# Optimization experiments

Measured on AMD Instinct MI355X. Metric: run time of the kernel, lower is better.

## Reference

```python
import jax, jax.numpy as jnp
import numpy as np

N_NODES = 100000
N_EDGES = 1600000
DIM = 3
HID = 128
BN_EPS = 1e-5


def _bn(x, g, b):
    # BatchNorm1d, training-mode batch statistics (biased variance, like torch)
    m = jnp.mean(x, axis=0)
    v = jnp.var(x, axis=0)
    return (x - m) * jax.lax.rsqrt(v + BN_EPS) * g + b


def _gin_mlp(h, w1, b1, g1, be1, w2, b2, g2, be2, w3, b3):
    # Linear -> BN -> ReLU -> (Dropout: identity in eval) -> Linear -> BN -> ReLU -> Linear
    h = jax.nn.relu(_bn(h @ w1 + b1, g1, be1))
    h = jax.nn.relu(_bn(h @ w2 + b2, g2, be2))
    return h @ w3 + b3


def _gin_conv(x, src, dst, eps, mlp_params):
    # GINConv: mlp((1+eps)*x_i + sum_{j->i} x_j); scatter-add over edge targets
    agg = jax.ops.segment_sum(x[src], dst, num_segments=N_NODES)
    return _gin_mlp((1.0 + eps) * x + agg, *mlp_params)


def setup_inputs() -> dict:
    key = jax.random.key(0)
    ks = jax.random.split(key, 32)

    def w(k, shape, scale=0.05):
        return jax.random.normal(k, shape, dtype=jnp.float32) * scale

    inp = {}
    inp["coords"] = jax.random.normal(ks[0], (N_NODES, DIM), dtype=jnp.float32)
    inp["edge_index"] = jax.random.randint(ks[1], (2, N_EDGES), 0, N_NODES, dtype=jnp.int32)

    # GIN layer 0 MLP (dim -> hid -> hid -> hid)
    inp["g0_w1"] = w(ks[2], (DIM, HID)); inp["g0_b1"] = jnp.zeros((HID,), jnp.float32)
    inp["g0_g1"] = jnp.ones((HID,), jnp.float32); inp["g0_be1"] = jnp.zeros((HID,), jnp.float32)
    inp["g0_w2"] = w(ks[3], (HID, HID)); inp["g0_b2"] = jnp.zeros((HID,), jnp.float32)
    inp["g0_g2"] = jnp.ones((HID,), jnp.float32); inp["g0_be2"] = jnp.zeros((HID,), jnp.float32)
    inp["g0_w3"] = w(ks[4], (HID, HID)); inp["g0_b3"] = jnp.zeros((HID,), jnp.float32)
    inp["eps0"] = jnp.zeros((), jnp.float32)
    inp["bn0_g"] = jnp.ones((HID,), jnp.float32); inp["bn0_b"] = jnp.zeros((HID,), jnp.float32)

    # GIN layer 1 MLP (hid -> hid -> hid -> hid)
    inp["g1_w1"] = w(ks[5], (HID, HID)); inp["g1_b1"] = jnp.zeros((HID,), jnp.float32)
    inp["g1_g1"] = jnp.ones((HID,), jnp.float32); inp["g1_be1"] = jnp.zeros((HID,), jnp.float32)
    inp["g1_w2"] = w(ks[6], (HID, HID)); inp["g1_b2"] = jnp.zeros((HID,), jnp.float32)
    inp["g1_g2"] = jnp.ones((HID,), jnp.float32); inp["g1_be2"] = jnp.zeros((HID,), jnp.float32)
    inp["g1_w3"] = w(ks[7], (HID, HID)); inp["g1_b3"] = jnp.zeros((HID,), jnp.float32)
    inp["eps1"] = jnp.zeros((), jnp.float32)
    inp["bn1_g"] = jnp.ones((HID,), jnp.float32); inp["bn1_b"] = jnp.zeros((HID,), jnp.float32)

    # decoder MLP: (2*hid+1) -> hid -> hid//2 -> 1, sigmoid
    inp["d_w1"] = w(ks[8], (2 * HID + 1, HID)); inp["d_b1"] = jnp.zeros((HID,), jnp.float32)
    inp["d_g"] = jnp.ones((HID,), jnp.float32); inp["d_be"] = jnp.zeros((HID,), jnp.float32)
    inp["d_w2"] = w(ks[9], (HID, HID // 2)); inp["d_b2"] = jnp.zeros((HID // 2,), jnp.float32)
    inp["d_w3"] = w(ks[10], (HID // 2, 1)); inp["d_b3"] = jnp.zeros((1,), jnp.float32)
    return inp


def reference(coords, edge_index,
              g0_w1, g0_b1, g0_g1, g0_be1, g0_w2, g0_b2, g0_g2, g0_be2, g0_w3, g0_b3, eps0, bn0_g, bn0_b,
              g1_w1, g1_b1, g1_g1, g1_be1, g1_w2, g1_b2, g1_g2, g1_be2, g1_w3, g1_b3, eps1, bn1_g, bn1_b,
              d_w1, d_b1, d_g, d_be, d_w2, d_b2, d_w3, d_b3):
    node_0 = edge_index[0]
    node_1 = edge_index[1]

    mlp0 = (g0_w1, g0_b1, g0_g1, g0_be1, g0_w2, g0_b2, g0_g2, g0_be2, g0_w3, g0_b3)
    mlp1 = (g1_w1, g1_b1, g1_g1, g1_be1, g1_w2, g1_b2, g1_g2, g1_be2, g1_w3, g1_b3)

    x = _gin_conv(coords, node_0, node_1, eps0, mlp0)
    x = jax.nn.relu(_bn(x, bn0_g, bn0_b))
    x = _gin_conv(x, node_0, node_1, eps1, mlp1)
    x = jax.nn.relu(_bn(x, bn1_g, bn1_b))

    # edge_l_cntr branch: per-edge contour-length feature + endpoint concat
    l = jnp.linalg.norm(coords[node_1] - coords[node_0], axis=1, keepdims=True)  # [E,1]
    h = jnp.concatenate([x[node_0], x[node_1], l], axis=-1)  # [E, 2*hid+1]

    h = jax.nn.relu(_bn(h @ d_w1 + d_b1, d_g, d_be))
    h = jax.nn.relu(h @ d_w2 + d_b2)
    out = jax.nn.sigmoid((h @ d_w3 + d_b3).squeeze(-1))  # [E]
    return out
```

## Files before the change

kernel.cpp:

```cpp
#include <hip/hip_runtime.h>
#include <hip/hip_bf16.h>
#include <math.h>


typedef __attribute__((ext_vector_type(8))) __bf16 bf16x8;
typedef __attribute__((ext_vector_type(4))) float f32x4;

__device__ __forceinline__ unsigned int pack_bf16(float a, float b) {
    unsigned short ua = __builtin_bit_cast(unsigned short, __float2bfloat16(a));
    unsigned short ub = __builtin_bit_cast(unsigned short, __float2bfloat16(b));
    return (unsigned int)ua | ((unsigned int)ub << 16);
}


__global__ void hist_dst(const int* __restrict__ edst, int* __restrict__ cursor, int E) {
    int e = blockIdx.x * 256 + threadIdx.x;
    if (e < E) atomicAdd(&cursor[edst[e]], 1);
}

__global__ __launch_bounds__(1024) void scan_deg(const int* deg, int* rowoff, int* cursor, int N) {
    __shared__ int sums[1024];
    const int t = threadIdx.x;
    const int chunk = (N + 1023) >> 10;
    int lo = t * chunk, hi = lo + chunk;
    if (lo > N) lo = N;
    if (hi > N) hi = N;
    int s = 0;
    for (int i = lo; i < hi; ++i) s += deg[i];
    sums[t] = s;
    __syncthreads();
    for (int off = 1; off < 1024; off <<= 1) {
        int add = (t >= off) ? sums[t - off] : 0;
        __syncthreads();
        sums[t] += add;
        __syncthreads();
    }
    int run = sums[t] - s;
    for (int i = lo; i < hi; ++i) {
        int d = deg[i];
        rowoff[i] = run;
        cursor[i] = run;
        run += d;
    }
    if (t == 1023) rowoff[N] = sums[1023];
}

__global__ void fill_csr(const int* __restrict__ esrc, const int* __restrict__ edst,
                         const float* __restrict__ coords,
                         int* cursor, int* __restrict__ perm, int* __restrict__ dperm,
                         int* __restrict__ eperm, float* __restrict__ lperm, int E) {
    int e = blockIdx.x * 256 + threadIdx.x;
    if (e >= E) return;
    int s0 = esrc[e], d0 = edst[e];
    int pos = atomicAdd(&cursor[d0], 1);
    perm[pos] = s0;
    dperm[pos] = d0;
    eperm[pos] = e;
    float dx = coords[d0*3+0] - coords[s0*3+0];
    float dy = coords[d0*3+1] - coords[s0*3+1];
    float dz = coords[d0*3+2] - coords[s0*3+2];
    lperm[pos] = sqrtf(dx*dx + dy*dy + dz*dz);
}


__global__ void gather_coords(const float* __restrict__ coords,
                              const int* __restrict__ rowoff, const int* __restrict__ perm,
                              float* __restrict__ agg0, int N) {
    int i = blockIdx.x * 256 + threadIdx.x;
    if (i >= N) return;
    float ax = 0.f, ay = 0.f, az = 0.f;
    int b = rowoff[i], t = rowoff[i+1];
    for (int j = b; j < t; ++j) {
        int p = perm[j];
        ax += coords[p*3+0];
        ay += coords[p*3+1];
        az += coords[p*3+2];
    }
    agg0[i*3+0] = ax; agg0[i*3+1] = ay; agg0[i*3+2] = az;
}

__global__ __launch_bounds__(256) void gather_combine_bn(const float* __restrict__ x,
                                                         const int* __restrict__ rowoff,
                                                         const int* __restrict__ perm,
                                                         const float* __restrict__ sc,
                                                         const float* __restrict__ sh,
                                                         const float* __restrict__ eps,
                                                         float* __restrict__ y, int N) {
    int node = blockIdx.x * 4 + (threadIdx.x >> 6);
    int lane = threadIdx.x & 63;
    if (node >= N) return;
    float ep = 1.f + *eps;
    const float2* x2 = (const float2*)x;
    float2 scv = ((const float2*)sc)[lane];
    float2 shv = ((const float2*)sh)[lane];
    int b = rowoff[node], t = rowoff[node+1];
    float2 acc = make_float2(0.f, 0.f);
    int j = b;
    for (; j + 2 <= t; j += 2) {
        int p0 = perm[j], p1 = perm[j+1];
        float2 v0 = x2[(size_t)p0*64 + lane];
        float2 v1 = x2[(size_t)p1*64 + lane];
        acc.x += fmaxf(fmaf(v0.x, scv.x, shv.x), 0.f) + fmaxf(fmaf(v1.x, scv.x, shv.x), 0.f);
        acc.y += fmaxf(fmaf(v0.y, scv.y, shv.y), 0.f) + fmaxf(fmaf(v1.y, scv.y, shv.y), 0.f);
    }
    if (j < t) {
        int p = perm[j];
        float2 v = x2[(size_t)p*64 + lane];
        acc.x += fmaxf(fmaf(v.x, scv.x, shv.x), 0.f);
        acc.y += fmaxf(fmaf(v.y, scv.y, shv.y), 0.f);
    }
    float2 own = x2[(size_t)node*64 + lane];
    acc.x = fmaf(ep, fmaxf(fmaf(own.x, scv.x, shv.x), 0.f), acc.x);
    acc.y = fmaf(ep, fmaxf(fmaf(own.y, scv.y, shv.y), 0.f), acc.y);
    ((float2*)y)[(size_t)node*64 + lane] = acc;
}


__global__ __launch_bounds__(256) void lin0(const float* __restrict__ coords,
                                            const float* __restrict__ agg0,
                                            const float* __restrict__ W1,
                                            const float* __restrict__ b1,
                                            const float* __restrict__ eps0,
                                            float* __restrict__ t1,
                                            float* __restrict__ stats, int nrows) {
    int col = threadIdx.x & 127, half = threadIdx.x >> 7;
    float w0 = W1[col], w1 = W1[128+col], w2 = W1[256+col], bb = b1[col];
    float ep = 1.f + *eps0;
    float s = 0.f, q = 0.f;
    int r0 = blockIdx.x * 64;
    for (int i = 0; i < 32; ++i) {
        int row = r0 + half + 2*i;
        if (row < nrows) {
            float h0 = fmaf(ep, coords[row*3+0], agg0[row*3+0]);
            float h1 = fmaf(ep, coords[row*3+1], agg0[row*3+1]);
            float h2 = fmaf(ep, coords[row*3+2], agg0[row*3+2]);
            float v = fmaf(h0, w0, fmaf(h1, w1, fmaf(h2, w2, bb)));
            t1[row*128+col] = v;
            s += v; q += v*v;
        }
    }
    __shared__ float red[512];
    red[half*128+col] = s;
    red[256 + half*128+col] = q;
    __syncthreads();
    if (threadIdx.x < 128) {
        atomicAdd(&stats[col],       red[col] + red[128+col]);
        atomicAdd(&stats[128+col],   red[256+col] + red[384+col]);
    }
}

__global__ void bn_fin(const float* __restrict__ stats, const float* __restrict__ g,
                       const float* __restrict__ be, float* __restrict__ sc,
                       float* __restrict__ sh, float inv_count) {
    int c = threadIdx.x;
    float m = stats[c] * inv_count;
    float v = stats[128+c] * inv_count - m*m;
    float a = g[c] * rsqrtf(fmaxf(v, 0.f) + 1e-5f);
    sc[c] = a;
    sh[c] = be[c] - m*a;
}

__global__ void prep_w2(const float* __restrict__ W2, unsigned short* __restrict__ w2t) {
    int i = blockIdx.x * 256 + threadIdx.x;
    if (i >= 128*64) return;
    int k = i >> 6, c = i & 63;
    w2t[c*128 + k] = __builtin_bit_cast(unsigned short, __float2bfloat16(W2[i]));
}

__global__ void prep_wT(const float* __restrict__ w0, const float* __restrict__ w1,
                        const float* __restrict__ w2, const float* __restrict__ w3,
                        const float* __restrict__ w4, const float* __restrict__ w5,
                        const float* __restrict__ w6, unsigned short* __restrict__ dst) {
    int m = blockIdx.y;
    const float* src = (m==0)?w0:(m==1)?w1:(m==2)?w2:(m==3)?w3:(m==4)?w4:(m==5)?w5:w6;
    int i = blockIdx.x * 256 + threadIdx.x;
    int k = i >> 7, c = i & 127;
    dst[m*16384 + c*128 + k] =
        __builtin_bit_cast(unsigned short, __float2bfloat16(src[i]));
}

template<bool IN_BN, bool STATS>
__global__ __launch_bounds__(256) void gemm_mfma(const float* __restrict__ A,
                                                 const unsigned short* __restrict__ wT,
                                                 const float* __restrict__ bias,
                                                 const float* __restrict__ sc,
                                                 const float* __restrict__ sh,
                                                 float* __restrict__ C,
                                                 float* __restrict__ stats, int nrows) {
    __shared__ int4 sAi[1024];
    __shared__ int4 sBi[2048];
    __shared__ float sred[2][4][128];
    char* sA = (char*)sAi;
    char* sB = (char*)sBi;
    const int tid = threadIdx.x;
    const int tile0 = blockIdx.x * 64;

    {
        const int4* src = (const int4*)wT;
        #pragma unroll
        for (int ii = 0; ii < 8; ++ii) {
            int s = tid + 256*ii;
            int col = s >> 4, k16 = s & 15;
            int byte = ((col << 8) + (k16 << 4)) ^ ((col & 7) << 4);
            *(int4*)(sB + byte) = src[s];
        }
    }
    {
        const int c4 = tid & 31;
        const int rb = tid >> 5;
        float4 s4, t4;
        if (IN_BN) {
            s4 = ((const float4*)sc)[c4];
            t4 = ((const float4*)sh)[c4];
        }
        const float4* A4 = (const float4*)A;
        #pragma unroll
        for (int i = 0; i < 8; ++i) {
            int r = rb + 8*i;
            int row = tile0 + r;
            float4 v = make_float4(0.f, 0.f, 0.f, 0.f);
            if (row < nrows) {
                v = A4[(size_t)row*32 + c4];
                if (IN_BN) {
                    v.x = fmaxf(fmaf(v.x, s4.x, t4.x), 0.f);
                    v.y = fmaxf(fmaf(v.y, s4.y, t4.y), 0.f);
                    v.z = fmaxf(fmaf(v.z, s4.z, t4.z), 0.f);
                    v.w = fmaxf(fmaf(v.w, s4.w, t4.w), 0.f);
                }
            }
            uint2 pk;
            pk.x = pack_bf16(v.x, v.y);
            pk.y = pack_bf16(v.z, v.w);
            int byte = ((r << 8) + (c4 << 3)) ^ ((r & 7) << 4);
            *(uint2*)(sA + byte) = pk;
        }
    }
    __syncthreads();

    const int l = tid & 63;
    const int w = tid >> 6;
    const int arow = (w << 4) + (l & 15);
    const int kbase = (l >> 4) << 3;
    f32x4 accv[8];
    #pragma unroll
    for (int c = 0; c < 8; ++c) accv[c] = (f32x4){0.f, 0.f, 0.f, 0.f};

    #pragma unroll
    for (int t = 0; t < 4; ++t) {
        int k0 = t*32 + kbase;
        int abyte = ((arow << 8) + (k0 << 1)) ^ ((arow & 7) << 4);
        bf16x8 af = __builtin_bit_cast(bf16x8, *(const int4*)(sA + abyte));
        #pragma unroll
        for (int c = 0; c < 8; ++c) {
            int bcol = (c << 4) + (l & 15);
            int bbyte = ((bcol << 8) + (k0 << 1)) ^ ((bcol & 7) << 4);
            bf16x8 bf = __builtin_bit_cast(bf16x8, *(const int4*)(sB + bbyte));
            accv[c] = __builtin_amdgcn_mfma_f32_16x16x32_bf16(af, bf, accv[c], 0, 0, 0);
        }
    }

    const int rj = (l >> 4) << 2;
    float lsum[8], lsq[8];
    #pragma unroll
    for (int c = 0; c < 8; ++c) {
        int col = (c << 4) + (l & 15);
        float bv = bias ? bias[col] : 0.f;
        f32x4 a = accv[c];
        float s = 0.f, q = 0.f;
        #pragma unroll
        for (int j = 0; j < 4; ++j) {
            int row = tile0 + (w << 4) + rj + j;
            float o = a[j] + bv;
            if (row < nrows) {
                C[(size_t)row*128 + col] = o;
                if (STATS) { s += o; q += o*o; }
            }
        }
        lsum[c] = s; lsq[c] = q;
    }
    if (STATS) {
        #pragma unroll
        for (int c = 0; c < 8; ++c) {
            lsum[c] += __shfl_xor(lsum[c], 16, 64);
            lsum[c] += __shfl_xor(lsum[c], 32, 64);
            lsq[c]  += __shfl_xor(lsq[c], 16, 64);
            lsq[c]  += __shfl_xor(lsq[c], 32, 64);
        }
        if ((l >> 4) == 0) {
            #pragma unroll
            for (int c = 0; c < 8; ++c) {
                int col = (c << 4) + l;
                sred[0][w][col] = lsum[c];
                sred[1][w][col] = lsq[c];
            }
        }
        __syncthreads();
        if (tid < 128) {
            float s = sred[0][0][tid] + sred[0][1][tid] + sred[0][2][tid] + sred[0][3][tid];
            float q = sred[1][0][tid] + sred[1][1][tid] + sred[1][2][tid] + sred[1][3][tid];
            atomicAdd(&stats[tid], s);
            atomicAdd(&stats[128 + tid], q);
        }
    }
}

__global__ __launch_bounds__(256) void csr_stats(const float* __restrict__ ya,
                                                 const float* __restrict__ yb,
                                                 const int* __restrict__ rowoff,
                                                 const int* __restrict__ perm,
                                                 const float* __restrict__ lperm,
                                                 const float* __restrict__ wl,
                                                 const float* __restrict__ b1,
                                                 float* __restrict__ stats, int N, int nspan) {
    int w = blockIdx.x * 4 + (threadIdx.x >> 6);
    int lane = threadIdx.x & 63;
    const float2* ya2 = (const float2*)ya;
    const float2* yb2 = (const float2*)yb;
    float2 wl2 = ((const float2*)wl)[lane];
    float2 b12 = ((const float2*)b1)[lane];
    float2 s = make_float2(0.f, 0.f), q = make_float2(0.f, 0.f);
    int i0 = w * nspan;
    int i1 = i0 + nspan; if (i1 > N) i1 = N;
    for (int i = i0; i < i1; ++i) {
        float2 ybr = yb2[(size_t)i*64 + lane];
        int b = rowoff[i], t = rowoff[i+1];
        for (int j = b; j < t; ++j) {
            int p = perm[j];
            float lv = lperm[j];
            float2 a = ya2[(size_t)p*64 + lane];
            float zx = a.x + ybr.x + fmaf(lv, wl2.x, b12.x);
            float zy = a.y + ybr.y + fmaf(lv, wl2.y, b12.y);
            s.x += zx; s.y += zy;
            q.x += zx*zx; q.y += zy*zy;
        }
    }
    __shared__ float red[1024];
    int wv = threadIdx.x >> 6;
    red[wv*128 + lane*2]       = s.x;
    red[wv*128 + lane*2 + 1]   = s.y;
    red[512 + wv*128 + lane*2]     = q.x;
    red[512 + wv*128 + lane*2 + 1] = q.y;
    __syncthreads();
    if (threadIdx.x < 128) {
        int c = threadIdx.x;
        float ss = red[c] + red[128+c] + red[256+c] + red[384+c];
        float qq = red[512+c] + red[640+c] + red[768+c] + red[896+c];
        atomicAdd(&stats[c], ss);
        atomicAdd(&stats[128+c], qq);
    }
}

__global__ __launch_bounds__(256) void decoder_fused(const float* __restrict__ ya,
                                                     const float* __restrict__ yb,
                                                     const float* __restrict__ lperm,
                                                     const int* __restrict__ perm,
                                                     const int* __restrict__ dperm,
                                                     const int* __restrict__ eperm,
                                                     const float* __restrict__ wl,
                                                     const float* __restrict__ b1,
                                                     const float* __restrict__ sc,
                                                     const float* __restrict__ sh,
                                                     const unsigned short* __restrict__ w2t,
                                                     const float* __restrict__ b2,
                                                     const float* __restrict__ w3,
                                                     const float* __restrict__ b3p,
                                                     float* __restrict__ out, int E) {
    __shared__ int4 sAB[2048];
    char* sA = (char*)sAB;
    char* sB = (char*)sAB + 16384;
    const int tid = threadIdx.x;
    const int tile0 = blockIdx.x * 64;

    {
        const int4* src = (const int4*)w2t;
        #pragma unroll
        for (int ii = 0; ii < 4; ++ii) {
            int s = tid + 256*ii;
            int col = s >> 4, k16 = s & 15;
            int byte = ((col << 8) + (k16 << 4)) ^ ((col & 7) << 4);
            *(int4*)(sB + byte) = src[s];
        }
    }
    {
        const int c4 = tid & 31;
        const int rb = tid >> 5;
        float4 wv = ((const float4*)wl)[c4];
        float4 bb = ((const float4*)b1)[c4];
        float4 s4 = ((const float4*)sc)[c4];
        float4 t4 = ((const float4*)sh)[c4];
        #pragma unroll
        for (int i = 0; i < 8; ++i) {
            int r = rb + 8*i;
            int row = tile0 + r;
            float4 v = make_float4(0.f, 0.f, 0.f, 0.f);
            if (row < E) {
                int s0 = perm[row], d0 = dperm[row];
                float lv = lperm[row];
                float4 va = ((const float4*)ya)[(size_t)s0*32 + c4];
                float4 vb = ((const float4*)yb)[(size_t)d0*32 + c4];
                v.x = fmaxf(fmaf(va.x + vb.x + fmaf(lv, wv.x, bb.x), s4.x, t4.x), 0.f);
                v.y = fmaxf(fmaf(va.y + vb.y + fmaf(lv, wv.y, bb.y), s4.y, t4.y), 0.f);
                v.z = fmaxf(fmaf(va.z + vb.z + fmaf(lv, wv.z, bb.z), s4.z, t4.z), 0.f);
                v.w = fmaxf(fmaf(va.w + vb.w + fmaf(lv, wv.w, bb.w), s4.w, t4.w), 0.f);
            }
            uint2 pk;
            pk.x = pack_bf16(v.x, v.y);
            pk.y = pack_bf16(v.z, v.w);
            int byte = ((r << 8) + (c4 << 3)) ^ ((r & 7) << 4);
            *(uint2*)(sA + byte) = pk;
        }
    }
    __syncthreads();

    const int l = tid & 63;
    const int w = tid >> 6;
    const int arow = (w << 4) + (l & 15);
    const int kbase = (l >> 4) << 3;
    f32x4 accv[4];
    #pragma unroll
    for (int c = 0; c < 4; ++c) accv[c] = (f32x4){0.f, 0.f, 0.f, 0.f};

    #pragma unroll
    for (int t = 0; t < 4; ++t) {
        int k0 = t*32 + kbase;
        int abyte = ((arow << 8) + (k0 << 1)) ^ ((arow & 7) << 4);
        bf16x8 af = __builtin_bit_cast(bf16x8, *(const int4*)(sA + abyte));
        #pragma unroll
        for (int c = 0; c < 4; ++c) {
            int bcol = (c << 4) + (l & 15);
            int bbyte = ((bcol << 8) + (k0 << 1)) ^ ((bcol & 7) << 4);
            bf16x8 bf = __builtin_bit_cast(bf16x8, *(const int4*)(sB + bbyte));
            accv[c] = __builtin_amdgcn_mfma_f32_16x16x32_bf16(af, bf, accv[c], 0, 0, 0);
        }
    }

    float p0 = 0.f, p1 = 0.f, p2 = 0.f, p3 = 0.f;
    #pragma unroll
    for (int c = 0; c < 4; ++c) {
        int col = (c << 4) + (l & 15);
        float b2c = b2[col], w3c = w3[col];
        f32x4 a = accv[c];
        p0 = fmaf(fmaxf(a[0] + b2c, 0.f), w3c, p0);
        p1 = fmaf(fmaxf(a[1] + b2c, 0.f), w3c, p1);
        p2 = fmaf(fmaxf(a[2] + b2c, 0.f), w3c, p2);
        p3 = fmaf(fmaxf(a[3] + b2c, 0.f), w3c, p3);
    }
    #pragma unroll
    for (int m = 1; m < 16; m <<= 1) {
        p0 += __shfl_xor(p0, m, 64);
        p1 += __shfl_xor(p1, m, 64);
        p2 += __shfl_xor(p2, m, 64);
        p3 += __shfl_xor(p3, m, 64);
    }
    if ((l & 15) == 0) {
        float b3v = b3p[0];
        int rbase = tile0 + (w << 4) + ((l >> 4) << 2);
        float pj[4] = {p0, p1, p2, p3};
        #pragma unroll
        for (int j = 0; j < 4; ++j) {
            int row = rbase + j;
            if (row < E) out[eperm[row]] = 1.f / (1.f + expf(-(pj[j] + b3v)));
        }
    }
}


extern "C" void kernel_launch(void* const* d_in, const int* in_sizes, int n_in,
                              void* d_out, int out_size, void* d_ws, size_t ws_size,
                              hipStream_t stream) {
    const int N = in_sizes[0] / 3;
    const int E = in_sizes[1] / 2;

    const float* coords = (const float*)d_in[0];
    const int*   ei     = (const int*)d_in[1];
    const int*   esrc = ei;
    const int*   edst = ei + E;
    const float* g0_w1 = (const float*)d_in[2];
    const float* g0_b1 = (const float*)d_in[3];
    const float* g0_g1 = (const float*)d_in[4];
    const float* g0_be1= (const float*)d_in[5];
    const float* g0_w2 = (const float*)d_in[6];
    const float* g0_b2 = (const float*)d_in[7];
    const float* g0_g2 = (const float*)d_in[8];
    const float* g0_be2= (const float*)d_in[9];
    const float* g0_w3 = (const float*)d_in[10];
    const float* g0_b3 = (const float*)d_in[11];
    const float* eps0  = (const float*)d_in[12];
    const float* bn0_g = (const float*)d_in[13];
    const float* bn0_b = (const float*)d_in[14];
    const float* g1_w1 = (const float*)d_in[15];
    const float* g1_b1 = (const float*)d_in[16];
    const float* g1_g1 = (const float*)d_in[17];
    const float* g1_be1= (const float*)d_in[18];
    const float* g1_w2 = (const float*)d_in[19];
    const float* g1_b2 = (const float*)d_in[20];
    const float* g1_g2 = (const float*)d_in[21];
    const float* g1_be2= (const float*)d_in[22];
    const float* g1_w3 = (const float*)d_in[23];
    const float* g1_b3 = (const float*)d_in[24];
    const float* eps1  = (const float*)d_in[25];
    const float* bn1_g = (const float*)d_in[26];
    const float* bn1_b = (const float*)d_in[27];
    const float* d_w1  = (const float*)d_in[28];
    const float* d_b1  = (const float*)d_in[29];
    const float* d_g   = (const float*)d_in[30];
    const float* d_be  = (const float*)d_in[31];
    const float* d_w2  = (const float*)d_in[32];
    const float* d_b2  = (const float*)d_in[33];
    const float* d_w3  = (const float*)d_in[34];
    const float* d_b3  = (const float*)d_in[35];

    float* ws = (float*)d_ws;
    const size_t NF = (size_t)N * 128;
    float* buf0 = ws;
    float* buf1 = ws + NF;
    float* buf2 = ws + 2*NF;
    float* agg0 = ws + 3*NF;
    float* stats= agg0 + (size_t)N*3;
    float* scsh = stats + 7*256;
    float* lperm = scsh + 7*256;
    int*   cursor = (int*)(lperm + E);
    int*   rowoff = cursor + N;
    int*   perm   = rowoff + N + 1;
    int*   dperm  = perm + E;
    int*   eperm  = dperm + E;
    unsigned short* w2t = (unsigned short*)(eperm + E);
    unsigned short* wT  = w2t + 64*128;

    float* out = (float*)d_out;

    const float* wl = d_w1 + 256*128;

    #define STATSK(k) (stats + (k)*256)
    #define SC(k) (scsh + (k)*256)
    #define SH(k) (scsh + (k)*256 + 128)
    #define WT(m) (wT + (m)*16384)

    const int rowTiles = (N + 63) / 64;
    const int edgeTiles = (E + 63) / 64;
    const int eBlocks = (E + 255) / 256;
    const float invN = 1.f / (float)N;
    const float invE = 1.f / (float)E;
    const int nWaves = 2048 * 4;
    const int nspan = (N + nWaves - 1) / nWaves;

    hipMemsetAsync(stats, 0, 7*256 * sizeof(float), stream);
    hipMemsetAsync(cursor, 0, (size_t)N * sizeof(int), stream);

    hist_dst<<<eBlocks, 256, 0, stream>>>(edst, cursor, E);
    scan_deg<<<1, 1024, 0, stream>>>(cursor, rowoff, cursor, N);
    fill_csr<<<eBlocks, 256, 0, stream>>>(esrc, edst, coords, cursor, perm, dperm, eperm, lperm, E);
    prep_w2<<<32, 256, 0, stream>>>(d_w2, w2t);
    prep_wT<<<dim3(64, 7), 256, 0, stream>>>(g0_w2, g0_w3, g1_w1, g1_w2, g1_w3,
                                             d_w1, d_w1 + 128*128, wT);

    gather_coords<<<(N + 255)/256, 256, 0, stream>>>(coords, rowoff, perm, agg0, N);
    lin0<<<rowTiles, 256, 0, stream>>>(coords, agg0, g0_w1, g0_b1, eps0, buf0, STATSK(0), N);
    bn_fin<<<1, 128, 0, stream>>>(STATSK(0), g0_g1, g0_be1, SC(0), SH(0), invN);
    gemm_mfma<true,true><<<rowTiles, 256, 0, stream>>>(buf0, WT(0), g0_b2, SC(0), SH(0), buf1, STATSK(1), N);
    bn_fin<<<1, 128, 0, stream>>>(STATSK(1), g0_g2, g0_be2, SC(1), SH(1), invN);
    gemm_mfma<true,true><<<rowTiles, 256, 0, stream>>>(buf1, WT(1), g0_b3, SC(1), SH(1), buf2, STATSK(2), N);
    bn_fin<<<1, 128, 0, stream>>>(STATSK(2), bn0_g, bn0_b, SC(2), SH(2), invN);

    gather_combine_bn<<<(N + 3)/4, 256, 0, stream>>>(buf2, rowoff, perm, SC(2), SH(2), eps1, buf0, N);
    gemm_mfma<false,true><<<rowTiles, 256, 0, stream>>>(buf0, WT(2), g1_b1, nullptr, nullptr, buf1, STATSK(3), N);
    bn_fin<<<1, 128, 0, stream>>>(STATSK(3), g1_g1, g1_be1, SC(3), SH(3), invN);
    gemm_mfma<true,true><<<rowTiles, 256, 0, stream>>>(buf1, WT(3), g1_b2, SC(3), SH(3), buf2, STATSK(4), N);
    bn_fin<<<1, 128, 0, stream>>>(STATSK(4), g1_g2, g1_be2, SC(4), SH(4), invN);
    gemm_mfma<true,true><<<rowTiles, 256, 0, stream>>>(buf2, WT(4), g1_b3, SC(4), SH(4), buf0, STATSK(5), N);
    bn_fin<<<1, 128, 0, stream>>>(STATSK(5), bn1_g, bn1_b, SC(5), SH(5), invN);

    gemm_mfma<true,false><<<rowTiles, 256, 0, stream>>>(buf0, WT(5), nullptr, SC(5), SH(5), buf1, nullptr, N);
    gemm_mfma<true,false><<<rowTiles, 256, 0, stream>>>(buf0, WT(6), nullptr, SC(5), SH(5), buf2, nullptr, N);
    csr_stats<<<2048, 256, 0, stream>>>(buf1, buf2, rowoff, perm, lperm, wl, d_b1, STATSK(6), N, nspan);
    bn_fin<<<1, 128, 0, stream>>>(STATSK(6), d_g, d_be, SC(6), SH(6), invE);
    decoder_fused<<<edgeTiles, 256, 0, stream>>>(buf1, buf2, lperm, perm, dperm, eperm, wl, d_b1,
                                                 SC(6), SH(6), w2t, d_b2, d_w3, d_b3, out, E);
}
```

Measured before the change: 1.537 ms.

## Fold BN finalize into consumer kernels and store decoder node projections as bf16

Removes the separate bn_fin launches. Each consumer kernel (gemm, gather_combine_bn, decoder) now computes the BatchNorm scale and shift from the accumulated stats itself, which saves seven small serial kernel launches. The two decoder node-projection GEMMs now write bf16 instead of fp32, which halves the bytes csr_stats and decoder_fused read in their per-edge random gathers. The cost is redundant per-block stats math and lower precision in the decoder's first-layer inputs.

New measurement: 1.512 ms. About the same (-1.7%).

```diff
diff --git a/kernel.cpp b/kernel.cpp
--- a/kernel.cpp
+++ b/kernel.cpp
@@ -10,6 +10,12 @@
     unsigned short ua = __builtin_bit_cast(unsigned short, __float2bfloat16(a));
     unsigned short ub = __builtin_bit_cast(unsigned short, __float2bfloat16(b));
     return (unsigned int)ua | ((unsigned int)ub << 16);
+}
+__device__ __forceinline__ float bflo(unsigned int u) {
+    return __builtin_bit_cast(float, u << 16);
+}
+__device__ __forceinline__ float bfhi(unsigned int u) {
+    return __builtin_bit_cast(float, u & 0xffff0000u);
 }
 
 
@@ -82,26 +88,33 @@
 __global__ __launch_bounds__(256) void gather_combine_bn(const float* __restrict__ x,
                                                          const int* __restrict__ rowoff,
                                                          const int* __restrict__ perm,
-                                                         const float* __restrict__ sc,
-                                                         const float* __restrict__ sh,
+                                                         const float* __restrict__ st,
+                                                         const float* __restrict__ g,
+                                                         const float* __restrict__ be,
+                                                         float invN,
                                                          const float* __restrict__ eps,
                                                          float* __restrict__ y, int N) {
     int node = blockIdx.x * 4 + (threadIdx.x >> 6);
     int lane = threadIdx.x & 63;
     if (node >= N) return;
     float ep = 1.f + *eps;
+    int c0 = lane*2, c1 = c0 + 1;
+    float m0 = st[c0]*invN, m1 = st[c1]*invN;
+    float v0 = fmaxf(st[128+c0]*invN - m0*m0, 0.f);
+    float v1 = fmaxf(st[128+c1]*invN - m1*m1, 0.f);
+    float a0 = g[c0]*rsqrtf(v0 + 1e-5f), a1 = g[c1]*rsqrtf(v1 + 1e-5f);
+    float2 scv = make_float2(a0, a1);
+    float2 shv = make_float2(be[c0] - m0*a0, be[c1] - m1*a1);
     const float2* x2 = (const float2*)x;
-    float2 scv = ((const float2*)sc)[lane];
-    float2 shv = ((const float2*)sh)[lane];
     int b = rowoff[node], t = rowoff[node+1];
     float2 acc = make_float2(0.f, 0.f);
     int j = b;
     for (; j + 2 <= t; j += 2) {
         int p0 = perm[j], p1 = perm[j+1];
-        float2 v0 = x2[(size_t)p0*64 + lane];
-        float2 v1 = x2[(size_t)p1*64 + lane];
-        acc.x += fmaxf(fmaf(v0.x, scv.x, shv.x), 0.f) + fmaxf(fmaf(v1.x, scv.x, shv.x), 0.f);
-        acc.y += fmaxf(fmaf(v0.y, scv.y, shv.y), 0.f) + fmaxf(fmaf(v1.y, scv.y, shv.y), 0.f);
+        float2 v0v = x2[(size_t)p0*64 + lane];
+        float2 v1v = x2[(size_t)p1*64 + lane];
+        acc.x += fmaxf(fmaf(v0v.x, scv.x, shv.x), 0.f) + fmaxf(fmaf(v1v.x, scv.x, shv.x), 0.f);
+        acc.y += fmaxf(fmaf(v0v.y, scv.y, shv.y), 0.f) + fmaxf(fmaf(v1v.y, scv.y, shv.y), 0.f);
     }
     if (j < t) {
         int p = perm[j];
@@ -149,17 +162,6 @@
     }
 }
 
-__global__ void bn_fin(const float* __restrict__ stats, const float* __restrict__ g,
-                       const float* __restrict__ be, float* __restrict__ sc,
-                       float* __restrict__ sh, float inv_count) {
-    int c = threadIdx.x;
-    float m = stats[c] * inv_count;
-    float v = stats[128+c] * inv_count - m*m;
-    float a = g[c] * rsqrtf(fmaxf(v, 0.f) + 1e-5f);
-    sc[c] = a;
-    sh[c] = be[c] - m*a;
-}
-
 __global__ void prep_w2(const float* __restrict__ W2, unsigned short* __restrict__ w2t) {
     int i = blockIdx.x * 256 + threadIdx.x;
     if (i >= 128*64) return;
@@ -179,21 +181,37 @@
         __builtin_bit_cast(unsigned short, __float2bfloat16(src[i]));
 }
 
-template<bool IN_BN, bool STATS>
+template<bool IN_BN, bool STATS, bool OUT_BF16>
 __global__ __launch_bounds__(256) void gemm_mfma(const float* __restrict__ A,
                                                  const unsigned short* __restrict__ wT,
                                                  const float* __restrict__ bias,
-                                                 const float* __restrict__ sc,
-                                                 const float* __restrict__ sh,
+                                                 const float* __restrict__ inst,
+                                                 const float* __restrict__ bng,
+                                                 const float* __restrict__ bnb,
+                                                 float invCnt,
                                                  float* __restrict__ C,
+                                                 unsigned short* __restrict__ Cb,
                                                  float* __restrict__ stats, int nrows) {
     __shared__ int4 sAi[1024];
     __shared__ int4 sBi[2048];
     __shared__ float sred[2][4][128];
     char* sA = (char*)sAi;
     char* sB = (char*)sBi;
+    float* sSC = &sred[0][0][0];
+    float* sSH = &sred[0][1][0];
     const int tid = threadIdx.x;
     const int tile0 = blockIdx.x * 64;
+
+    if (IN_BN) {
+        if (tid < 128) {
+            float m = inst[tid] * invCnt;
+            float v = fmaxf(inst[128+tid] * invCnt - m*m, 0.f);
+            float a = bng[tid] * rsqrtf(v + 1e-5f);
+            sSC[tid] = a;
+            sSH[tid] = bnb[tid] - m*a;
+        }
+        __syncthreads();
+    }
 
     {
         const int4* src = (const int4*)wT;
@@ -210,8 +228,8 @@
         const int rb = tid >> 5;
         float4 s4, t4;
         if (IN_BN) {
-            s4 = ((const float4*)sc)[c4];
-            t4 = ((const float4*)sh)[c4];
+            s4 = ((const float4*)sSC)[c4];
+            t4 = ((const float4*)sSH)[c4];
         }
         const float4* A4 = (const float4*)A;
         #pragma unroll
@@ -272,7 +290,11 @@
             int row = tile0 + (w << 4) + rj + j;
             float o = a[j] + bv;
             if (row < nrows) {
-                C[(size_t)row*128 + col] = o;
+                if (OUT_BF16)
+                    Cb[(size_t)row*128 + col] =
+                        __builtin_bit_cast(unsigned short, __float2bfloat16(o));
+                else
+                    C[(size_t)row*128 + col] = o;
                 if (STATS) { s += o; q += o*o; }
             }
         }
@@ -286,6 +308,7 @@
             lsq[c]  += __shfl_xor(lsq[c], 16, 64);
             lsq[c]  += __shfl_xor(lsq[c], 32, 64);
         }
+        __syncthreads();
         if ((l >> 4) == 0) {
             #pragma unroll
             for (int c = 0; c < 8; ++c) {
@@ -304,8 +327,8 @@
     }
 }
 
-__global__ __launch_bounds__(256) void csr_stats(const float* __restrict__ ya,
-                                                 const float* __restrict__ yb,
+__global__ __launch_bounds__(256) void csr_stats(const unsigned short* __restrict__ ya,
+                                                 const unsigned short* __restrict__ yb,
                                                  const int* __restrict__ rowoff,
                                                  const int* __restrict__ perm,
                                                  const float* __restrict__ lperm,
@@ -314,22 +337,23 @@
                                                  float* __restrict__ stats, int N, int nspan) {
     int w = blockIdx.x * 4 + (threadIdx.x >> 6);
     int lane = threadIdx.x & 63;
-    const float2* ya2 = (const float2*)ya;
-    const float2* yb2 = (const float2*)yb;
+    const unsigned int* ya2 = (const unsigned int*)ya;
+    const unsigned int* yb2 = (const unsigned int*)yb;
     float2 wl2 = ((const float2*)wl)[lane];
     float2 b12 = ((const float2*)b1)[lane];
     float2 s = make_float2(0.f, 0.f), q = make_float2(0.f, 0.f);
     int i0 = w * nspan;
     int i1 = i0 + nspan; if (i1 > N) i1 = N;
     for (int i = i0; i < i1; ++i) {
-        float2 ybr = yb2[(size_t)i*64 + lane];
+        unsigned int ub = yb2[(size_t)i*64 + lane];
+        float ybx = bflo(ub), yby = bfhi(ub);
         int b = rowoff[i], t = rowoff[i+1];
         for (int j = b; j < t; ++j) {
             int p = perm[j];
             float lv = lperm[j];
-            float2 a = ya2[(size_t)p*64 + lane];
-            float zx = a.x + ybr.x + fmaf(lv, wl2.x, b12.x);
-            float zy = a.y + ybr.y + fmaf(lv, wl2.y, b12.y);
+            unsigned int ua = ya2[(size_t)p*64 + lane];
+            float zx = bflo(ua) + ybx + fmaf(lv, wl2.x, b12.x);
+            float zy = bfhi(ua) + yby + fmaf(lv, wl2.y, b12.y);
             s.x += zx; s.y += zy;
             q.x += zx*zx; q.y += zy*zy;
         }
@@ -350,16 +374,18 @@
     }
 }
 
-__global__ __launch_bounds__(256) void decoder_fused(const float* __restrict__ ya,
-                                                     const float* __restrict__ yb,
+__global__ __launch_bounds__(256) void decoder_fused(const unsigned short* __restrict__ ya,
+                                                     const unsigned short* __restrict__ yb,
                                                      const float* __restrict__ lperm,
                                                      const int* __restrict__ perm,
                                                      const int* __restrict__ dperm,
                                                      const int* __restrict__ eperm,
                                                      const float* __restrict__ wl,
                                                      const float* __restrict__ b1,
-                                                     const float* __restrict__ sc,
-                                                     const float* __restrict__ sh,
+                                                     const float* __restrict__ st6,
+                                                     const float* __restrict__ dg,
+                                                     const float* __restrict__ dbe,
+                                                     float invE,
                                                      const unsigned short* __restrict__ w2t,
                                                      const float* __restrict__ b2,
                                                      const float* __restrict__ w3,
@@ -386,8 +412,20 @@
         const int rb = tid >> 5;
         float4 wv = ((const float4*)wl)[c4];
         float4 bb = ((const float4*)b1)[c4];
-        float4 s4 = ((const float4*)sc)[c4];
-        float4 t4 = ((const float4*)sh)[c4];
+        float4 s4, t4;
+        {
+            int cb = c4 * 4;
+            #pragma unroll
+            for (int j = 0; j < 4; ++j) {
+                float m = st6[cb+j] * invE;
+                float v = fmaxf(st6[128+cb+j] * invE - m*m, 0.f);
+                float a = dg[cb+j] * rsqrtf(v + 1e-5f);
+                ((float*)&s4)[j] = a;
+                ((float*)&t4)[j] = dbe[cb+j] - m*a;
+            }
+        }
+        const uint2* ya2 = (const uint2*)ya;
+        const uint2* yb2 = (const uint2*)yb;
         #pragma unroll
         for (int i = 0; i < 8; ++i) {
             int r = rb + 8*i;
@@ -396,12 +434,14 @@
             if (row < E) {
                 int s0 = perm[row], d0 = dperm[row];
                 float lv = lperm[row];
-                float4 va = ((const float4*)ya)[(size_t)s0*32 + c4];
-                float4 vb = ((const float4*)yb)[(size_t)d0*32 + c4];
-                v.x = fmaxf(fmaf(va.x + vb.x + fmaf(lv, wv.x, bb.x), s4.x, t4.x), 0.f);
-                v.y = fmaxf(fmaf(va.y + vb.y + fmaf(lv, wv.y, bb.y), s4.y, t4.y), 0.f);
-                v.z = fmaxf(fmaf(va.z + vb.z + fmaf(lv, wv.z, bb.z), s4.z, t4.z), 0.f);
-                v.w = fmaxf(fmaf(va.w + vb.w + fmaf(lv, wv.w, bb.w), s4.w, t4.w), 0.f);
+                uint2 ua = ya2[(size_t)s0*32 + c4];
+                uint2 ubv = yb2[(size_t)d0*32 + c4];
+                float vax = bflo(ua.x), vay = bfhi(ua.x), vaz = bflo(ua.y), vaw = bfhi(ua.y);
+                float vbx = bflo(ubv.x), vby = bfhi(ubv.x), vbz = bflo(ubv.y), vbw = bfhi(ubv.y);
+                v.x = fmaxf(fmaf(vax + vbx + fmaf(lv, wv.x, bb.x), s4.x, t4.x), 0.f);
+                v.y = fmaxf(fmaf(vay + vby + fmaf(lv, wv.y, bb.y), s4.y, t4.y), 0.f);
+                v.z = fmaxf(fmaf(vaz + vbz + fmaf(lv, wv.z, bb.z), s4.z, t4.z), 0.f);
+                v.w = fmaxf(fmaf(vaw + vbw + fmaf(lv, wv.w, bb.w), s4.w, t4.w), 0.f);
             }
             uint2 pk;
             pk.x = pack_bf16(v.x, v.y);
@@ -526,14 +566,14 @@
     int*   eperm  = dperm + E;
     unsigned short* w2t = (unsigned short*)(eperm + E);
     unsigned short* wT  = w2t + 64*128;
+    unsigned short* ya_bf = (unsigned short*)buf1;
+    unsigned short* yb_bf = (unsigned short*)buf2;
 
     float* out = (float*)d_out;
 
     const float* wl = d_w1 + 256*128;
 
     #define STATSK(k) (stats + (k)*256)
-    #define SC(k) (scsh + (k)*256)
-    #define SH(k) (scsh + (k)*256 + 128)
     #define WT(m) (wT + (m)*16384)
 
     const int rowTiles = (N + 63) / 64;
@@ -556,24 +596,27 @@
 
     gather_coords<<<(N + 255)/256, 256, 0, stream>>>(coords, rowoff, perm, agg0, N);
     lin0<<<rowTiles, 256, 0, stream>>>(coords, agg0, g0_w1, g0_b1, eps0, buf0, STATSK(0), N);
-    bn_fin<<<1, 128, 0, stream>>>(STATSK(0), g0_g1, g0_be1, SC(0), SH(0), invN);
-    gemm_mfma<true,true><<<rowTiles, 256, 0, stream>>>(buf0, WT(0), g0_b2, SC(0), SH(0), buf1, STATSK(1), N);
-    bn_fin<<<1, 128, 0, stream>>>(STATSK(1), g0_g2, g0_be2, SC(1), SH(1), invN);
-    gemm_mfma<true,true><<<rowTiles, 256, 0, stream>>>(buf1, WT(1), g0_b3, SC(1), SH(1), buf2, STATSK(2), N);
-    bn_fin<<<1, 128, 0, stream>>>(STATSK(2), bn0_g, bn0_b, SC(2), SH(2), invN);
-
-    gather_combine_bn<<<(N + 3)/4, 256, 0, stream>>>(buf2, rowoff, perm, SC(2), SH(2), eps1, buf0, N);
-    gemm_mfma<false,true><<<rowTiles, 256, 0, stream>>>(buf0, WT(2), g1_b1, nullptr, nullptr, buf1, STATSK(3), N);
-    bn_fin<<<1, 128, 0, stream>>>(STATSK(3), g1_g1, g1_be1, SC(3), SH(3), invN);
-    gemm_mfma<true,true><<<rowTiles, 256, 0, stream>>>(buf1, WT(3), g1_b2, SC(3), SH(3), buf2, STATSK(4), N);
-    bn_fin<<<1, 128, 0, stream>>>(STATSK(4), g1_g2, g1_be2, SC(4), SH(4), invN);
-    gemm_mfma<true,true><<<rowTiles, 256, 0, stream>>>(buf2, WT(4), g1_b3, SC(4), SH(4), buf0, STATSK(5), N);
-    bn_fin<<<1, 128, 0, stream>>>(STATSK(5), bn1_g, bn1_b, SC(5), SH(5), invN);
-
-    gemm_mfma<true,false><<<rowTiles, 256, 0, stream>>>(buf0, WT(5), nullptr, SC(5), SH(5), buf1, nullptr, N);
-    gemm_mfma<true,false><<<rowTiles, 256, 0, stream>>>(buf0, WT(6), nullptr, SC(5), SH(5), buf2, nullptr, N);
-    csr_stats<<<2048, 256, 0, stream>>>(buf1, buf2, rowoff, perm, lperm, wl, d_b1, STATSK(6), N, nspan);
-    bn_fin<<<1, 128, 0, stream>>>(STATSK(6), d_g, d_be, SC(6), SH(6), invE);
-    decoder_fused<<<edgeTiles, 256, 0, stream>>>(buf1, buf2, lperm, perm, dperm, eperm, wl, d_b1,
-                                                 SC(6), SH(6), w2t, d_b2, d_w3, d_b3, out, E);
-}
+    gemm_mfma<true,true,false><<<rowTiles, 256, 0, stream>>>(
+        buf0, WT(0), g0_b2, STATSK(0), g0_g1, g0_be1, invN, buf1, nullptr, STATSK(1), N);
+    gemm_mfma<true,true,false><<<rowTiles, 256, 0, stream>>>(
+        buf1, WT(1), g0_b3, STATSK(1), g0_g2, g0_be2, invN, buf2, nullptr, STATSK(2), N);
+
+    gather_combine_bn<<<(N + 3)/4, 256, 0, stream>>>(
+        buf2, rowoff, perm, STATSK(2), bn0_g, bn0_b, invN, eps1, buf0, N);
+    gemm_mfma<false,true,false><<<rowTiles, 256, 0, stream>>>(
+        buf0, WT(2), g1_b1, nullptr, nullptr, nullptr, 0.f, buf1, nullptr, STATSK(3), N);
+    gemm_mfma<true,true,false><<<rowTiles, 256, 0, stream>>>(
+        buf1, WT(3), g1_b2, STATSK(3), g1_g1, g1_be1, invN, buf2, nullptr, STATSK(4), N);
+    gemm_mfma<true,true,false><<<rowTiles, 256, 0, stream>>>(
+        buf2, WT(4), g1_b3, STATSK(4), g1_g2, g1_be2, invN, buf0, nullptr, STATSK(5), N);
+
+    gemm_mfma<true,false,true><<<rowTiles, 256, 0, stream>>>(
+        buf0, WT(5), nullptr, STATSK(5), bn1_g, bn1_b, invN, nullptr, ya_bf, nullptr, N);
+    gemm_mfma<true,false,true><<<rowTiles, 256, 0, stream>>>(
+        buf0, WT(6), nullptr, STATSK(5), bn1_g, bn1_b, invN, nullptr, yb_bf, nullptr, N);
+    csr_stats<<<2048, 256, 0, stream>>>(ya_bf, yb_bf, rowoff, perm, lperm, wl, d_b1,
+                                        STATSK(6), N, nspan);
+    decoder_fused<<<edgeTiles, 256, 0, stream>>>(ya_bf, yb_bf, lperm, perm, dperm, eperm,
+                                                 wl, d_b1, STATSK(6), d_g, d_be, invE,
+                                                 w2t, d_b2, d_w3, d_b3, out, E);
+}
```
